# Optimization experiments

Hardware: AMD Instinct MI355X
Metric: run time of the kernel (lower is better)

The kernel has to match this reference:

```python
import jax, jax.numpy as jnp
import numpy as np

WINDOW = 32


def _dilate(mask, iters=5):
    # scipy binary_dilation with default cross structure, `iters` iterations
    m = mask.copy()
    for _ in range(iters):
        d = m.copy()
        d[1:, :] |= m[:-1, :]
        d[:-1, :] |= m[1:, :]
        d[:, 1:] |= m[:, :-1]
        d[:, :-1] |= m[:, 1:]
        m = d
    return m


def _label8(mask):
    # skimage measure.label, default 8-connectivity, via min-label propagation
    h, w = mask.shape
    lab = np.where(mask, np.arange(1, mask.size + 1, dtype=np.int64).reshape(h, w), 0)
    BIG = mask.size + 2
    while True:
        p = np.pad(np.where(mask, lab, BIG), 1, constant_values=BIG)
        m = np.full((h, w), BIG, dtype=np.int64)
        for dy in (-1, 0, 1):
            for dx in (-1, 0, 1):
                m = np.minimum(m, p[1 + dy:1 + dy + h, 1 + dx:1 + dx + w])
        new = np.where(mask, m, 0)
        if np.array_equal(new, lab):
            break
        lab = new
    u = np.unique(lab)
    out = np.searchsorted(u, lab)
    if u[0] != 0:
        out = out + 1
    return out


def _malis(seg_flat, e1, e2, costs, pos):
    # MALIS edge weights: Kruskal on descending affinities with union-find;
    # pos=True counts same-(nonzero)-label pairs merged by each edge,
    # pos=False counts cross-label pairs between labeled nodes.
    n = seg_flat.size
    parent = np.arange(n)
    cnt = [dict() for _ in range(n)]
    for i in range(n):
        s = int(seg_flat[i])
        if s != 0:
            cnt[i][s] = 1
    w = np.zeros(costs.shape[0], np.float32)

    def find(x):
        r = x
        while parent[r] != r:
            r = parent[r]
        while parent[x] != r:
            parent[x], x = r, parent[x]
        return r

    order = np.argsort(-costs, kind='stable')
    for ei in order:
        ra, rb = find(int(e1[ei])), find(int(e2[ei]))
        if ra == rb:
            continue
        ca, cb = cnt[ra], cnt[rb]
        small, large = (ca, cb) if len(ca) <= len(cb) else (cb, ca)
        same = 0
        for kk, v in small.items():
            same += v * large.get(kk, 0)
        if pos:
            w[ei] = same
        else:
            sa = sum(ca.values())
            sb = sum(cb.values())
            w[ei] = sa * sb - same
        parent[rb] = ra
        for kk, v in cb.items():
            ca[kk] = ca.get(kk, 0) + v
        cnt[rb] = None
    return w


def compute_malis_weights(pred_np, target_np):
    B, C, H, W = pred_np.shape
    wn_full = np.zeros(pred_np.shape, np.float32)
    wp_full = np.zeros(pred_np.shape, np.float32)
    win = WINDOW
    idx = np.arange(win * win).reshape(win, win)
    e1 = np.concatenate([idx[:, :-1].ravel(), idx[:-1, :].ravel()])
    e2 = np.concatenate([idx[:, 1:].ravel(), idx[1:, :].ravel()])
    for k in range(H // win):
        for j in range(W // win):
            p = pred_np[:, :, k * win:(k + 1) * win, j * win:(j + 1) * win]
            t = target_np[:, :, k * win:(k + 1) * win, j * win:(j + 1) * win]
            costs = np.concatenate([
                (p[:, :, :, :-1] + p[:, :, :, 1:]).reshape(B, -1),
                (p[:, :, :-1, :] + p[:, :, 1:, :]).reshape(B, -1)], axis=1).astype(np.float32)
            gtc = np.concatenate([
                (t[:, :, :, :-1] + t[:, :, :, 1:]).reshape(B, -1),
                (t[:, :, :-1, :] + t[:, :, 1:, :]).reshape(B, -1)], axis=1).astype(np.float32)
            costs_n = costs.copy()
            costs_p = costs.copy()
            costs_n[gtc > 20] = 20
            costs_p[gtc < 10] = 0
            gtc = np.minimum(gtc, 20)
            for i in range(B):
                sg = _label8(_dilate(t[i, 0] == 0, 5) == 0)
                en = _malis(sg.ravel(), e1, e2, costs_n[i], False)
                ep = _malis(sg.ravel(), e1, e2, costs_p[i], True)
                sn = en.sum()
                if sn > 0:
                    en = en / sn
                sp = ep.sum()
                if sp > 0:
                    ep = ep / sp
                en[gtc[i] >= 10] = 0
                ep[gtc[i] < 20] = 0
                for ew, out in ((en, wn_full), (ep, wp_full)):
                    wh, wv = np.split(ew, 2)
                    wh = wh.reshape(win, win - 1)
                    wv = wv.reshape(win - 1, win)
                    nodes = np.zeros((win, win), np.float32)
                    nodes[:, :-1] += wh
                    nodes[:, 1:] += wh
                    nodes[:-1, :] += wv
                    nodes[1:, :] += wv
                    out[i, 0, k * win:(k + 1) * win, j * win:(j + 1) * win] = nodes
    return wn_full, wp_full


def setup_inputs() -> dict:
    key = jax.random.key(0)
    k1, k2 = jax.random.split(key)
    pred = jax.random.uniform(k1, (2, 1, 256, 256), jnp.float32) * 20.0
    target = jax.random.randint(k2, (2, 1, 256, 256), 0, 26).astype(jnp.float32)
    return {"pred": pred, "target": target, "malis_lr": 1.0, "malis_lr_pos": 1.0}


def reference(pred, target, malis_lr, malis_lr_pos):
    # weights are computed from detached values (CPU graph algorithm), constants wrt autodiff
    wn, wp = compute_malis_weights(np.asarray(pred), np.asarray(target))
    wn = jnp.asarray(wn, jnp.float32)
    wp = jnp.asarray(wp, jnp.float32)
    loss = malis_lr * jnp.square(pred) * wn + malis_lr_pos * jnp.square(20.0 - pred) * wp
    return loss.sum()
```

## Files before the change

### kernel.cpp

```cpp
#include <hip/hip_runtime.h>
#include <cstdint>

#define NPIX  1024
#define NH    992
#define NEDGE 1984
#define NSORT 2048
#define NGRP  31
#define HFS   4300
#define POOLN (NPIX + 2*HFS)

typedef unsigned long long u64;
typedef unsigned int u32;

static __device__ __forceinline__ u64 packRoot(int sL,int off,int len,int cap){
    return (u64)(u32)(sL & 0x7FF) | ((u64)(u32)(off & 0x3FFF) << 11) |
           ((u64)(u32)(len & 0x7FF) << 25) | ((u64)(u32)(cap & 0x7FF) << 36);
}
#define R_SL(R)  ((int)((R) & 0x7FF))
#define R_OFF(R) ((int)(((R)>>11) & 0x3FFF))
#define R_LEN(R) ((int)(((R)>>25) & 0x7FF))
#define R_CAP(R) ((int)(((R)>>36) & 0x7FF))

static __device__ __forceinline__ int rdl(int v, int l){ return __builtin_amdgcn_readlane(v, l); }

static __device__ __forceinline__ u64 sxor64(u64 v, int m){
    u32 lo = (u32)__shfl_xor((int)(v & 0xFFFFFFFFull), m, 64);
    u32 hi = (u32)__shfl_xor((int)(v >> 32), m, 64);
    return ((u64)hi << 32) | lo;
}

static __device__ __forceinline__ void edgeAB(int e, int &a, int &b){
    if (e < NH) { int r = (int)((unsigned)e / 31u); a = e + r; b = a + 1; }
    else        { a = e - NH; b = a + 32; }
}

#define CE(x, y, up) { u64 _a=(x), _b=(y); bool _lt=(_a<_b); \
    u64 _mn=_lt?_a:_b, _mx=_lt?_b:_a; (x)=(up)?_mn:_mx; (y)=(up)?_mx:_mn; }
#define CEX(x, xm, keepmin) { u64 _p=sxor64((x),(xm)); bool _lt=((x)<_p); \
    u64 _mn=_lt?(x):_p, _mx=_lt?_p:(x); (x)=(keepmin)?_mn:_mx; }

static __device__ __forceinline__ int wredi(int v){
    #pragma unroll
    for (int o = 32; o > 0; o >>= 1) v += __shfl_xor(v, o, 64);
    return v;
}
static __device__ __forceinline__ float wredf(float v){
    #pragma unroll
    for (int o = 32; o > 0; o >>= 1) v += __shfl_xor(v, o, 64);
    return v;
}

__global__ __launch_bounds__(128) void malis_kernel(
    const float* __restrict__ pred,
    const float* __restrict__ target,
    const float* __restrict__ lr_p,
    const float* __restrict__ lrp_p,
    float* __restrict__ out)
{
    const int tid  = threadIdx.x;
    const int lane = tid & 63;
    const int wv   = tid >> 6;
    const int bid  = blockIdx.x;
    const int bb   = bid >> 6;
    const int win  = bid & 63;
    const int wy   = win >> 3, wx = win & 7;
    const int base = bb * 65536 + (wy * 32) * 256 + wx * 32;

    __shared__ __align__(16) u32 Ks[2][NSORT];
    __shared__ u64   root[2][NPIX];
    __shared__ float predL[NPIX];
    __shared__ float costs[NEDGE];
    __shared__ u32   poolS[2][POOLN];
    __shared__ u32   Q[2][NPIX];
    __shared__ float Qw[2][NPIX];
    __shared__ short seg[NPIX];
    __shared__ short par[2][NPIX];
    __shared__ short H[2][NPIX + 1];
    __shared__ unsigned char tgtL[NPIX];
    __shared__ unsigned char gtcL[NEDGE];
    __shared__ int   flags[2];

    unsigned char* mA    = (unsigned char*)poolS;
    unsigned char* mB    = mA + NPIX;
    short*         labId = (short*)(mA + 2 * NPIX);

    for (int i = tid; i < NPIX; i += 128) {
        int r = i >> 5, c = i & 31;
        float pv = pred[base + r * 256 + c];
        float tv = target[base + r * 256 + c];
        predL[i] = pv;
        tgtL[i]  = (unsigned char)tv;
        mA[i]    = (tv == 0.0f) ? 1 : 0;
    }
    if (tid == 0) flags[1] = 0;
    __syncthreads();

    unsigned char* srcm = mA;
    unsigned char* dstm = mB;
    for (int it = 0; it < 5; ++it) {
        for (int i = tid; i < NPIX; i += 128) {
            int r = i >> 5, c = i & 31;
            unsigned char v = srcm[i];
            if (r > 0)  v |= srcm[i - 32];
            if (r < 31) v |= srcm[i + 32];
            if (c > 0)  v |= srcm[i - 1];
            if (c < 31) v |= srcm[i + 1];
            dstm[i] = v;
        }
        __syncthreads();
        unsigned char* t2 = srcm; srcm = dstm; dstm = t2;
    }

    for (int i = tid; i < NPIX; i += 128)
        seg[i] = srcm[i] ? (short)-1 : (short)i;
    __syncthreads();

    for (;;) {
        if (tid == 0) flags[0] = 0;
        __syncthreads();
        bool any = false;
        for (int i = tid; i < NPIX; i += 128) {
            int cur = seg[i];
            if (cur < 0) continue;
            int r = i >> 5, c = i & 31;
            int m = cur;
            if (r > 0) {
                if (c > 0)  { int t = seg[i - 33]; if (t >= 0 && t < m) m = t; }
                { int t = seg[i - 32]; if (t >= 0 && t < m) m = t; }
                if (c < 31) { int t = seg[i - 31]; if (t >= 0 && t < m) m = t; }
            }
            if (c > 0)  { int t = seg[i - 1]; if (t >= 0 && t < m) m = t; }
            if (c < 31) { int t = seg[i + 1]; if (t >= 0 && t < m) m = t; }
            if (r < 31) {
                if (c > 0)  { int t = seg[i + 31]; if (t >= 0 && t < m) m = t; }
                { int t = seg[i + 32]; if (t >= 0 && t < m) m = t; }
                if (c < 31) { int t = seg[i + 33]; if (t >= 0 && t < m) m = t; }
            }
            #pragma unroll
            for (int t2 = 0; t2 < 6; ++t2) {
                int s2 = seg[m];
                if (s2 >= 0 && s2 < m) m = s2; else break;
            }
            if (m < cur) { seg[i] = (short)m; any = true; }
        }
        if (any) flags[0] = 1;
        __syncthreads();
        if (flags[0] == 0) break;
        __syncthreads();
    }

    for (int i = tid; i < NPIX; i += 128)
        if (seg[i] == (short)i) labId[i] = (short)atomicAdd(&flags[1], 1);
    __syncthreads();
    for (int i = tid; i < NPIX; i += 128) {
        short s2 = seg[i];
        seg[i] = (s2 < 0) ? (short)0 : (short)(labId[s2] + 1);
    }

    for (int e = tid; e < NEDGE; e += 128) {
        int a, b2; edgeAB(e, a, b2);
        costs[e] = predL[a] + predL[b2];
        gtcL[e]  = (unsigned char)(tgtL[a] + tgtL[b2]);
    }
    __syncthreads();

    const int ph = wv;
    u32*   Ks_   = Ks[ph];
    short* par_  = par[ph];
    u64*   root_ = root[ph];
    u32*   pool_ = poolS[ph];
    short* H_    = H[ph];
    u32*   Q_    = Q[ph];
    float* Qw_   = Qw[ph];
    u32*   claim_= (u32*)Qw[ph];

    u64 sk[32];
    #pragma unroll
    for (int r = 0; r < 32; ++r) {
        int e = lane * 32 + r;
        u64 kv = ~0ULL;
        if (e < NEDGE) {
            float cv = costs[e];
            int g = gtcL[e];
            if (ph == 0) { if (g > 20) cv = 20.0f; }
            else         { if (g < 10) cv = 0.0f; }
            kv = (((u64)(~__float_as_uint(cv))) << 32) | (u32)e;
        }
        sk[r] = kv;
    }
    #pragma unroll
    for (int kk2 = 2; kk2 <= 32; kk2 <<= 1) {
        #pragma unroll
        for (int j = kk2 >> 1; j > 0; j >>= 1) {
            #pragma unroll
            for (int r = 0; r < 32; ++r) {
                if ((r & j) == 0) {
                    bool up = (kk2 == 32) ? ((lane & 1) == 0) : ((r & kk2) == 0);
                    CE(sk[r], sk[r | j], up);
                }
            }
        }
    }
    #pragma unroll
    for (int kk2 = 64; kk2 <= 2048; kk2 <<= 1) {
        const bool up = ((lane & (kk2 >> 5)) == 0);
        #pragma unroll
        for (int j = kk2 >> 1; j >= 32; j >>= 1) {
            const int xm = j >> 5;
            const bool keepmin = (((lane & xm) == 0) == up);
            #pragma unroll
            for (int r = 0; r < 32; ++r) { CEX(sk[r], xm, keepmin); }
        }
        #pragma unroll
        for (int j = 16; j > 0; j >>= 1) {
            #pragma unroll
            for (int r = 0; r < 32; ++r) {
                if ((r & j) == 0) { CE(sk[r], sk[r | j], up); }
            }
        }
    }
    #pragma unroll
    for (int r = 0; r < 32; r += 4) {
        uint4 v4;
        v4.x = (u32)sk[r]; v4.y = (u32)sk[r+1]; v4.z = (u32)sk[r+2]; v4.w = (u32)sk[r+3];
        *(uint4*)&Ks_[lane * 32 + r] = v4;
    }

    for (int i = lane; i < NPIX; i += 64) {
        short s2 = seg[i];
        par_[i] = (short)(i | (s2 ? 0x8000 : 0));
        if (s2) {
            root_[i] = packRoot(1, i, 1, 1);
            pool_[i] = ((u32)(unsigned short)s2 << 16) | 1u;
        } else {
            root_[i] = 0;
        }
        H_[i] = 0;
        claim_[i] = ~0u;
    }
    if (lane == 0) H_[NPIX] = 0;
    __builtin_amdgcn_wave_barrier();

    int qn = 0;
    u32 rnd = 1;
    const u64 ltm = (1ull << lane) - 1;
    int curE = (int)Ks_[lane];
    for (int g2 = 0; g2 < NGRP; ++g2) {
        int nextE = (g2 + 1 < NGRP) ? (int)Ks_[(g2 + 1) * 64 + lane] : 0;
        const int myE = curE;
        int ea, eb2; edgeAB(myE, ea, eb2);
        int ra = ea, rb = eb2;
        int laA, laB;
        for (;;) {
            int va = (int)(unsigned short)par_[ra];
            int vb = (int)(unsigned short)par_[rb];
            int pa = va & 0x3FF, pb = vb & 0x3FF;
            bool fa = (pa != ra), fb = (pb != rb);
            if (!fa && !fb) { laA = va >> 15; laB = vb >> 15; break; }
            int ga = (int)(unsigned short)par_[pa];
            int gb = (int)(unsigned short)par_[pb];
            if (fa) { par_[ra] = (short)ga; ra = ga & 0x3FF; }
            if (fb) { par_[rb] = (short)gb; rb = gb & 0x3FF; }
        }
        bool alive = (ra != rb);

        for (;;) {
            if (!__ballot(alive)) break;
            const bool av = alive;
            const u32 tag = ((0x03FFFFFFu - rnd) << 6) | (u32)lane;
            ++rnd;
            int mn = ra < rb ? ra : rb;
            int mx = ra < rb ? rb : ra;
            int winner = (laA == laB) ? mn : (laA ? ra : rb);
            int loser  = (laA == laB) ? mx : (laA ? rb : ra);
            bool wgt = (laA & laB) != 0;
            if (av)        atomicMin(&claim_[loser],  tag);
            if (av && wgt) atomicMin(&claim_[winner], tag);
            bool sel = false;
            if (av) {
                u32 cl = claim_[loser];
                u32 cw = wgt ? claim_[winner] : tag;
                sel = (cl == tag) && (cw == tag);
            }
            u64 wm = __ballot(sel && wgt);
            if (sel && wgt) Q_[qn + __popcll(wm & ltm)] =
                (u32)myE | ((u32)mn << 11) | ((u32)mx << 21);
            qn += (int)__popcll(wm);
            if (sel) par_[loser] = (short)winner;
            if (av) {
                for (;;) {
                    int va = (int)(unsigned short)par_[ra];
                    int vb = (int)(unsigned short)par_[rb];
                    int pa = va & 0x3FF, pb = vb & 0x3FF;
                    bool fa = (pa != ra), fb = (pb != rb);
                    if (!fa && !fb) { laA = va >> 15; laB = vb >> 15; break; }
                    int ga = (int)(unsigned short)par_[pa];
                    int gb = (int)(unsigned short)par_[pb];
                    if (fa) { par_[ra] = (short)ga; ra = ga & 0x3FF; }
                    if (fb) { par_[rb] = (short)gb; rb = gb & 0x3FF; }
                }
                alive = !sel && (ra != rb);
            }
        }
        curE = nextE;
        __builtin_amdgcn_wave_barrier();
    }

    u32 bump = NPIX;
    u32 halfEnd = NPIX + HFS;
    int curHalf = 0;

    auto do_gc = [&]() {
        u32 tgt = (curHalf == 0) ? (u32)(NPIX + HFS) : (u32)NPIX;
        u32 nb = tgt;
        for (int c = 0; c < 16; ++c) {
            int i0 = c * 64 + lane;
            bool live = (root_[i0] != 0);
            u64 rbm = __ballot(live);
            while (rbm) {
                int j = __ffsll(rbm) - 1; rbm &= rbm - 1;
                int r = c * 64 + j;
                u64 R = root_[r];
                int len = R_LEN(R);
                int off = R_OFF(R);
                for (int t = lane; t < len; t += 64) {
                    u32 v2 = pool_[off + t];
                    pool_[nb + t] = v2;
                }
                __builtin_amdgcn_wave_barrier();
                if (lane == 0) root_[r] = packRoot(R_SL(R), (int)nb, len, len);
                nb += (u32)len;
            }
        }
        bump = nb;
        halfEnd = tgt + HFS;
        curHalf ^= 1;
    };

    for (int q = 0; q < qn; ++q) {
        u32 rec = Q_[q];
        int A  = (int)((rec >> 11) & 0x3FF);
        int B  = (int)((rec >> 21) & 0x3FF);
        int winner = A;
        int dead   = B;
        u64 RA = root_[A], RB = root_[B];
        int sLa = R_SL(RA), sLb = R_SL(RB);
        int lenA = R_LEN(RA), lenB = R_LEN(RB);
        if (bump + (u32)(lenA + lenB + 8) > halfEnd) {
            do_gc();
            RA = root_[A]; RB = root_[B];
            lenA = R_LEN(RA); lenB = R_LEN(RB);
        }
        int offA = R_OFF(RA), capA = R_CAP(RA);
        int offB = R_OFF(RB), capB = R_CAP(RB);
        int offS, lenS, offL, lenL, capL;
        if (lenA <= lenB) { offS = offA; lenS = lenA; offL = offB; lenL = lenB; capL = capB; }
        else              { offS = offB; lenS = lenB; offL = offA; lenL = lenA; capL = capA; }
        int same = 0, dOff, dLen, dCap;

        if (lenS + lenL <= 64) {
            u32 eL = (lane < lenL) ? pool_[offL + lane] : 0u;
            u32 eS = (lane < lenS) ? pool_[offS + lane] : 0u;
            dLen = lenL;
            for (int t = 0; t < lenS; ++t) {
                u32 xs = (u32)rdl((int)eS, t);
                bool match = (lane < lenL) && ((eL >> 16) == (xs >> 16));
                u64 mb = __ballot(match);
                if (mb) {
                    int ml = __ffsll(mb) - 1;
                    same += (int)(xs & 0xFFFF) * ((int)rdl((int)eL, ml) & 0xFFFF);
                    if (match) eL += (xs & 0xFFFF);
                } else {
                    if (lane == dLen) eL = xs;
                    dLen++;
                }
            }
            if (dLen <= capL) { dOff = offL; dCap = capL; }
            else { dOff = (int)bump; dCap = (dLen + 3) & ~3; bump += (u32)dCap; }
            if (lane < dLen) pool_[dOff + lane] = eL;
        } else {
            dOff = (int)bump;
            dCap = (lenL + lenS + 4) & ~3; bump += (u32)dCap;
            for (int j = lane; j < lenS; j += 64) {
                u32 es = pool_[offS + j];
                H_[es >> 16] = (short)(es & 0xFFFF);
            }
            __builtin_amdgcn_wave_barrier();
            int sp = 0;
            for (int j = lane; j < lenL; j += 64) {
                u32 el = pool_[offL + j];
                int h = (int)H_[el >> 16];
                sp += h * (int)(el & 0xFFFF);
                pool_[dOff + j] = el + (u32)h;
                if (h) H_[el >> 16] = 0;
            }
            same = wredi(sp);
            __builtin_amdgcn_wave_barrier();
            int baseU = 0;
            for (int j0 = 0; j0 < lenS; j0 += 64) {
                int j = j0 + lane;
                bool un = false; u32 es = 0;
                if (j < lenS) { es = pool_[offS + j]; un = (H_[es >> 16] != 0); }
                u64 ub = __ballot(un);
                if (un) {
                    int pos = __popcll(ub & ltm);
                    pool_[dOff + lenL + baseU + pos] = es;
                    H_[es >> 16] = 0;
                }
                baseU += __popcll(ub);
            }
            dLen = lenL + baseU;
        }
        if (lane == 0) {
            Qw_[q] = (float)(ph ? same : (sLa * sLb - same));
            root_[winner] = packRoot(sLa + sLb, dOff, dLen, dCap);
            root_[dead]   = 0;
        }
        __builtin_amdgcn_wave_barrier();
    }

    float s_loc = 0.0f;
    for (int q = lane; q < qn; q += 64) s_loc += Qw_[q];
    const float sn = wredf(s_loc);

    const float scale = ph ? lrp_p[0] : lr_p[0];
    float acc = 0.0f;
    for (int q = lane; q < qn; q += 64) {
        float wv2 = Qw_[q];
        if (wv2 == 0.0f) continue;
        if (sn > 0.0f) wv2 /= sn;
        int me = (int)(Q_[q] & 0x7FF);
        int g = gtcL[me];
        bool zero = ph ? (g < 20) : (g >= 10);
        if (zero) continue;
        int a2, b2; edgeAB(me, a2, b2);
        float pa = predL[a2], pb = predL[b2];
        float fa2, fb2;
        if (ph == 0) { fa2 = pa * pa; fb2 = pb * pb; }
        else { float qa = 20.0f - pa, qb = 20.0f - pb; fa2 = qa * qa; fb2 = qb * qb; }
        acc += scale * wv2 * (fa2 + fb2);
    }
    acc = wredf(acc);
    if (lane == 0) atomicAdd(out, acc);
}

__global__ void zero_out_kernel(float* o)
{
    if (threadIdx.x == 0 && blockIdx.x == 0) o[0] = 0.0f;
}

extern "C" void kernel_launch(void* const* d_in, const int* in_sizes, int n_in,
                              void* d_out, int out_size, void* d_ws, size_t ws_size,
                              hipStream_t stream)
{
    const float* pred   = (const float*)d_in[0];
    const float* target = (const float*)d_in[1];
    const float* lr     = (const float*)d_in[2];
    const float* lrp    = (const float*)d_in[3];
    float* out = (float*)d_out;

    zero_out_kernel<<<1, 64, 0, stream>>>(out);
    malis_kernel<<<128, 128, 0, stream>>>(pred, target, lr, lrp, out);
}
```

Measured before the change: 374.8 us.

## Use bitmask dilation and run-based union-find for connected component labeling

Replaces per-pixel byte-mask dilation with 32-bit row bitmasks built by wave ballots and dilated by a single thread using shifts. Replaces iterative per-pixel min-label propagation with labeling over horizontal foreground runs, merged through atomicMin union-find with pointer jumping between iterations. The aim is fewer barrier-separated passes and less shared-memory traffic in the labeling prologue. Having one thread do the dilation serializes that step, and the atomic union-find is more intricate. Labels may be assigned in a different order, but only the partition into components is used afterward.

New measurement: 346.0 us. 1.08x faster.

```diff
diff --git a/kernel.cpp b/kernel.cpp
--- a/kernel.cpp
+++ b/kernel.cpp
@@ -78,83 +78,119 @@
     __shared__ short H[2][NPIX + 1];
     __shared__ unsigned char tgtL[NPIX];
     __shared__ unsigned char gtcL[NEDGE];
+    __shared__ u32   rowmaskL[32];
+    __shared__ u32   fgL[32];
+    __shared__ unsigned short baseL[33];
     __shared__ int   flags[2];
 
-    unsigned char* mA    = (unsigned char*)poolS;
-    unsigned char* mB    = mA + NPIX;
-    short*         labId = (short*)(mA + 2 * NPIX);
-
-    for (int i = tid; i < NPIX; i += 128) {
+    u32* runPar = (u32*)poolS;
+    unsigned short* labIdRun = (unsigned short*)(runPar + 512);
+
+    for (int j = 0; j < 8; ++j) {
+        int i = tid + 128 * j;
         int r = i >> 5, c = i & 31;
         float pv = pred[base + r * 256 + c];
         float tv = target[base + r * 256 + c];
         predL[i] = pv;
         tgtL[i]  = (unsigned char)tv;
-        mA[i]    = (tv == 0.0f) ? 1 : 0;
+        u64 zb = __ballot(tv == 0.0f);
+        if (lane == 0) {
+            int rr = 4 * j + 2 * wv;
+            rowmaskL[rr]     = (u32)zb;
+            rowmaskL[rr + 1] = (u32)(zb >> 32);
+        }
     }
     if (tid == 0) flags[1] = 0;
+    for (int x = tid; x < 512; x += 128) runPar[x] = (u32)x;
     __syncthreads();
 
-    unsigned char* srcm = mA;
-    unsigned char* dstm = mB;
-    for (int it = 0; it < 5; ++it) {
-        for (int i = tid; i < NPIX; i += 128) {
-            int r = i >> 5, c = i & 31;
-            unsigned char v = srcm[i];
-            if (r > 0)  v |= srcm[i - 32];
-            if (r < 31) v |= srcm[i + 32];
-            if (c > 0)  v |= srcm[i - 1];
-            if (c < 31) v |= srcm[i + 1];
-            dstm[i] = v;
-        }
-        __syncthreads();
-        unsigned char* t2 = srcm; srcm = dstm; dstm = t2;
-    }
-
-    for (int i = tid; i < NPIX; i += 128)
-        seg[i] = srcm[i] ? (short)-1 : (short)i;
+    if (tid == 0) {
+        u32 m0[32];
+        #pragma unroll
+        for (int r = 0; r < 32; ++r) m0[r] = rowmaskL[r];
+        #pragma unroll
+        for (int it = 0; it < 5; ++it) {
+            u32 d[32];
+            #pragma unroll
+            for (int r = 0; r < 32; ++r) {
+                u32 v = m0[r] | (m0[r] << 1) | (m0[r] >> 1);
+                if (r > 0)  v |= m0[r - 1];
+                if (r < 31) v |= m0[r + 1];
+                d[r] = v;
+            }
+            #pragma unroll
+            for (int r = 0; r < 32; ++r) m0[r] = d[r];
+        }
+        int acc = 0;
+        #pragma unroll
+        for (int r = 0; r < 32; ++r) {
+            u32 f = ~m0[r];
+            fgL[r] = f;
+            baseL[r] = (unsigned short)acc;
+            acc += __popc(f & ~(f << 1));
+        }
+        baseL[32] = (unsigned short)acc;
+    }
     __syncthreads();
+    const int nRuns = (int)baseL[32];
 
     for (;;) {
         if (tid == 0) flags[0] = 0;
         __syncthreads();
-        bool any = false;
-        for (int i = tid; i < NPIX; i += 128) {
-            int cur = seg[i];
-            if (cur < 0) continue;
+        bool chg = false;
+        for (int j = 0; j < 8; ++j) {
+            int i = tid + 128 * j;
             int r = i >> 5, c = i & 31;
-            int m = cur;
-            if (r > 0) {
-                if (c > 0)  { int t = seg[i - 33]; if (t >= 0 && t < m) m = t; }
-                { int t = seg[i - 32]; if (t >= 0 && t < m) m = t; }
-                if (c < 31) { int t = seg[i - 31]; if (t >= 0 && t < m) m = t; }
-            }
-            if (c > 0)  { int t = seg[i - 1]; if (t >= 0 && t < m) m = t; }
-            if (c < 31) { int t = seg[i + 1]; if (t >= 0 && t < m) m = t; }
-            if (r < 31) {
-                if (c > 0)  { int t = seg[i + 31]; if (t >= 0 && t < m) m = t; }
-                { int t = seg[i + 32]; if (t >= 0 && t < m) m = t; }
-                if (c < 31) { int t = seg[i + 33]; if (t >= 0 && t < m) m = t; }
-            }
-            #pragma unroll
-            for (int t2 = 0; t2 < 6; ++t2) {
-                int s2 = seg[m];
-                if (s2 >= 0 && s2 < m) m = s2; else break;
-            }
-            if (m < cur) { seg[i] = (short)m; any = true; }
-        }
-        if (any) flags[0] = 1;
+            if (r == 0) continue;
+            u32 fr = fgL[r];
+            if (!((fr >> c) & 1u)) continue;
+            u32 fu = fgL[r - 1];
+            u32 nb = fu & (u32)((7ull << c) >> 1);
+            if (!nb) continue;
+            u32 Sr = fr & ~(fr << 1);
+            int a = (int)baseL[r] + __popc(Sr & ((2u << c) - 1u)) - 1;
+            for (;;) { int p = (int)runPar[a]; if (p == a) break; a = p; }
+            u32 Su = fu & ~(fu << 1);
+            int bu = (int)baseL[r - 1];
+            while (nb) {
+                int cc = __ffs((int)nb) - 1; nb &= nb - 1;
+                int b = bu + __popc(Su & ((2u << cc) - 1u)) - 1;
+                for (;;) { int p = (int)runPar[b]; if (p == b) break; b = p; }
+                if (a != b) {
+                    int mnr = a < b ? a : b;
+                    int mxr = a ^ b ^ mnr;
+                    atomicMin(&runPar[mxr], (u32)mnr);
+                    chg = true;
+                    a = mnr;
+                }
+            }
+        }
+        if (chg) flags[0] = 1;
         __syncthreads();
-        if (flags[0] == 0) break;
+        if (!flags[0]) break;
+        for (int x = tid; x < nRuns; x += 128) {
+            u32 p = runPar[x];
+            runPar[x] = runPar[p];
+        }
         __syncthreads();
     }
 
-    for (int i = tid; i < NPIX; i += 128)
-        if (seg[i] == (short)i) labId[i] = (short)atomicAdd(&flags[1], 1);
+    for (int x = tid; x < nRuns; x += 128)
+        if ((int)runPar[x] == x) labIdRun[x] = (unsigned short)atomicAdd(&flags[1], 1);
     __syncthreads();
-    for (int i = tid; i < NPIX; i += 128) {
-        short s2 = seg[i];
-        seg[i] = (s2 < 0) ? (short)0 : (short)(labId[s2] + 1);
+
+    for (int j = 0; j < 8; ++j) {
+        int i = tid + 128 * j;
+        int r = i >> 5, c = i & 31;
+        u32 fr = fgL[r];
+        short s = 0;
+        if ((fr >> c) & 1u) {
+            u32 Sr = fr & ~(fr << 1);
+            int x = (int)baseL[r] + __popc(Sr & ((2u << c) - 1u)) - 1;
+            for (;;) { int p = (int)runPar[x]; if (p == x) break; x = p; }
+            s = (short)((int)labIdRun[x] + 1);
+        }
+        seg[i] = s;
     }
 
     for (int e = tid; e < NEDGE; e += 128) {
```
